# Kernel tuning notes

Hardware: AMD Instinct MI355X
Metric: run time of the kernel (lower is better)

## Reference

```python
import jax, jax.numpy as jnp
import numpy as np

B, H, W, C = 32, 56, 56, 192
WS, SHIFT, NH = 7, 3, 6
HD = C // NH
N = WS * WS
NW = (H // WS) * (W // WS)
HID = 4 * C
EPS = 1e-5


def _np_window_partition(x, ws):
    b, h, w, c = x.shape
    x = x.reshape(b, h // ws, ws, w // ws, ws, c)
    return x.transpose(0, 1, 3, 2, 4, 5).reshape(-1, ws * ws, c)


def build_attn_mask():
    img = np.zeros((1, H, W, 1), dtype=np.float32)
    cnt = 0
    for hs in (slice(0, -WS), slice(-WS, -SHIFT), slice(-SHIFT, None)):
        for ws_ in (slice(0, -WS), slice(-WS, -SHIFT), slice(-SHIFT, None)):
            img[:, hs, ws_, :] = cnt
            cnt += 1
    mw = _np_window_partition(img, WS).squeeze(-1)  # (nW, N)
    am = mw[:, None, :] - mw[:, :, None]
    am = np.where(am != 0, -100.0, 0.0).astype(np.float32)
    return jnp.asarray(am)  # (nW, N, N)


def layernorm(x, g, b):
    mu = jnp.mean(x, axis=-1, keepdims=True)
    var = jnp.var(x, axis=-1, keepdims=True)
    return (x - mu) * jax.lax.rsqrt(var + EPS) * g + b


def setup_inputs() -> dict:
    key = jax.random.key(0)
    ks = jax.random.split(key, 8)
    s = 0.02
    return {
        "x": jax.random.normal(ks[0], (B, H * W, C), dtype=jnp.float32),
        "qkv_w": jax.random.normal(ks[1], (C, 3 * C), dtype=jnp.float32) * s,
        "qkv_b": jnp.zeros((3 * C,), dtype=jnp.float32),
        "proj_w": jax.random.normal(ks[2], (C, C), dtype=jnp.float32) * s,
        "proj_b": jnp.zeros((C,), dtype=jnp.float32),
        "n1_g": jnp.ones((C,), dtype=jnp.float32),
        "n1_b": jnp.zeros((C,), dtype=jnp.float32),
        "n2_g": jnp.ones((C,), dtype=jnp.float32),
        "n2_b": jnp.zeros((C,), dtype=jnp.float32),
        "fc1_w": jax.random.normal(ks[3], (C, HID), dtype=jnp.float32) * s,
        "fc1_b": jnp.zeros((HID,), dtype=jnp.float32),
        "fc2_w": jax.random.normal(ks[4], (HID, C), dtype=jnp.float32) * s,
        "fc2_b": jnp.zeros((C,), dtype=jnp.float32),
        "attn_mask": build_attn_mask(),
    }


def reference(x, qkv_w, qkv_b, proj_w, proj_b, n1_g, n1_b, n2_g, n2_b,
              fc1_w, fc1_b, fc2_w, fc2_b, attn_mask):
    scale = HD ** -0.5
    xv = x.reshape(B, H, W, C)
    shifted = jnp.roll(xv, shift=(-SHIFT, -SHIFT), axis=(1, 2))
    # window partition -> (B*nW, N, C)
    wins = shifted.reshape(B, H // WS, WS, W // WS, WS, C)
    wins = wins.transpose(0, 1, 3, 2, 4, 5).reshape(-1, N, C)
    xn = layernorm(wins, n1_g, n1_b)
    qkv = (xn @ qkv_w + qkv_b).reshape(-1, N, 3, NH, HD)
    q, k, v = qkv[:, :, 0], qkv[:, :, 1], qkv[:, :, 2]  # (B_, N, NH, HD)
    attn = jnp.einsum('bnhd,bmhd->bhnm', q, k) * scale   # (B_, NH, N, N)
    attn = attn.reshape(B, NW, NH, N, N) + attn_mask[None, :, None]
    attn = jax.nn.softmax(attn.reshape(-1, NH, N, N), axis=-1)
    out = jnp.einsum('bhnm,bmhd->bnhd', attn, v).reshape(-1, N, C)
    out = out @ proj_w + proj_b
    # window reverse
    xr = out.reshape(B, H // WS, W // WS, WS, WS, C)
    xr = xr.transpose(0, 1, 3, 2, 4, 5).reshape(B, H, W, C)
    xr = jnp.roll(xr, shift=(SHIFT, SHIFT), axis=(1, 2)).reshape(B, H * W, C)
    # NOTE: no residual around attention (faithful to source); residual only on MLP
    h = layernorm(xr, n2_g, n2_b)
    mlp = jax.nn.gelu(h @ fc1_w + fc1_b, approximate=False) @ fc2_w + fc2_b
    return xr + mlp
```

## Files before the change

### kernel.cpp

```cpp
#include <hip/hip_runtime.h>

typedef unsigned short u16;
typedef unsigned int u32;
typedef __bf16 bf16x8 __attribute__((ext_vector_type(8)));
typedef float f32x4 __attribute__((ext_vector_type(4)));

#define MFMA16(a,b,c) __builtin_amdgcn_mfma_f32_16x16x32_bf16((a),(b),(c),0,0,0)

__device__ __forceinline__ u16 f2bf(float x) {
  u32 u = __float_as_uint(x);
  u32 r = (u + 0x7fffu + ((u >> 16) & 1u)) >> 16;
  return (u16)r;
}

__device__ __forceinline__ float gelu_f(float v) {
  float u = v * 0.70710678118654752f;
  float a = fabsf(u);
  float t = 1.f / (1.f + 0.3275911f * a);
  float p = t * (0.254829592f + t * (-0.284496736f + t * (1.421413741f +
            t * (-1.453152027f + t * 1.061405429f))));
  float e = __expf(-u * u);
  float er = 1.f - p * e;
  er = (u < 0.f) ? -er : er;
  return 0.5f * v * (1.f + er);
}

__global__ __launch_bounds__(256) void prep_weights(
    const float* __restrict__ qkv_w, const float* __restrict__ proj_w,
    const float* __restrict__ fc1_w, const float* __restrict__ fc2_w,
    u16* __restrict__ qkv_wf, u16* __restrict__ proj_wf,
    u16* __restrict__ fc1_wf, u16* __restrict__ fc2_wf) {
  int t0 = blockIdx.x * 256 + threadIdx.x;
  int stride = gridDim.x * 256;
  for (int i = t0; i < 36 * 6 * 512; i += stride) {
    int f = i >> 9, ln = (i >> 3) & 63, e = i & 7;
    int ct = f / 6, kc = f - ct * 6;
    int n = ct * 16 + (ln & 15), k = kc * 32 + (ln >> 4) * 8 + e;
    qkv_wf[i] = f2bf(qkv_w[k * 576 + n]);
  }
  for (int i = t0; i < 12 * 6 * 512; i += stride) {
    int f = i >> 9, ln = (i >> 3) & 63, e = i & 7;
    int ct = f / 6, kc = f - ct * 6;
    int n = ct * 16 + (ln & 15), k = kc * 32 + (ln >> 4) * 8 + e;
    proj_wf[i] = f2bf(proj_w[k * 192 + n]);
  }
  for (int i = t0; i < 48 * 6 * 512; i += stride) {
    int f = i >> 9, ln = (i >> 3) & 63, e = i & 7;
    int ctg = f / 6, kc = f - ctg * 6;
    int n = ctg * 16 + (ln & 15), k = kc * 32 + (ln >> 4) * 8 + e;
    fc1_wf[i] = f2bf(fc1_w[k * 768 + n]);
  }
  for (int i = t0; i < 24 * 12 * 512; i += stride) {
    int f = i >> 9, ln = (i >> 3) & 63, e = i & 7;
    int g2 = f / 12, ct = f - g2 * 12;
    int n = ct * 16 + (ln & 15), k = g2 * 32 + (ln >> 4) * 8 + e;
    fc2_wf[i] = f2bf(fc2_w[k * 192 + n]);
  }
}

__global__ __launch_bounds__(256) void qkv_ln_kernel(
    const float* __restrict__ x, const float* __restrict__ g,
    const float* __restrict__ bb,
    const u16* __restrict__ qkv_wf, const float* __restrict__ qkv_b,
    u16* __restrict__ qkvb, int rowbase, int wbase) {
  __shared__ __align__(16) u16 sA[128 * 200];
  const int tid = threadIdx.x;
  const int r0 = rowbase + blockIdx.x * 128;

  {
    int r = tid >> 1, half = tid & 1;
    int gr = r0 + r;
    int w = gr / 49, n = gr - w * 49;
    int b = w >> 6, wi = w & 63;
    int rr = n / 7, cc = n - rr * 7;
    int hh = (wi >> 3) * 7 + rr + 3; if (hh >= 56) hh -= 56;
    int ww = (wi & 7) * 7 + cc + 3; if (ww >= 56) ww -= 56;
    const float* src = x + ((size_t)b * 3136 + hh * 56 + ww) * 192 + half * 96;
    float s1 = 0.f, s2 = 0.f;
    #pragma unroll
    for (int i = 0; i < 24; i++) {
      float4 v = ((const float4*)src)[i];
      s1 += v.x + v.y + v.z + v.w;
      s2 += v.x * v.x + v.y * v.y + v.z * v.z + v.w * v.w;
    }
    s1 += __shfl_xor(s1, 1);
    s2 += __shfl_xor(s2, 1);
    float mu = s1 * (1.f / 192.f);
    float var = s2 * (1.f / 192.f) - mu * mu;
    float rs = rsqrtf(var + 1e-5f);
    u16* drow = sA + r * 200 + half * 96;
    #pragma unroll
    for (int i = 0; i < 24; i++) {
      float4 v = ((const float4*)src)[i];
      int c = half * 96 + i * 4;
      ushort4 o;
      o.x = f2bf((v.x - mu) * rs * g[c + 0] + bb[c + 0]);
      o.y = f2bf((v.y - mu) * rs * g[c + 1] + bb[c + 1]);
      o.z = f2bf((v.z - mu) * rs * g[c + 2] + bb[c + 2]);
      o.w = f2bf((v.w - mu) * rs * g[c + 3] + bb[c + 3]);
      *((ushort4*)(drow + i * 4)) = o;
    }
  }
  __syncthreads();

  const int wv = tid >> 6, ln = tid & 63, lrow = ln & 15, quad = ln >> 4;
  const int ln8 = ln << 3;

  u32 qkoff[8], voff[8];
  #pragma unroll
  for (int rt = 0; rt < 2; rt++) {
    #pragma unroll
    for (int reg = 0; reg < 4; reg++) {
      int grow = r0 + 32 * wv + 16 * rt + quad * 4 + reg;
      int w_ = grow / 49, n_ = grow - w_ * 49;
      u32 wb = (u32)(w_ - wbase) * 29568u;
      qkoff[rt * 4 + reg] = wb + (u32)n_ * 32u;
      voff[rt * 4 + reg] = wb + (u32)n_;
    }
  }

  for (int ct = 0; ct < 36; ct++) {
    f32x4 acc0 = (f32x4){0.f, 0.f, 0.f, 0.f};
    f32x4 acc1 = (f32x4){0.f, 0.f, 0.f, 0.f};
    #pragma unroll
    for (int kc = 0; kc < 6; kc++) {
      bf16x8 a0 = *(const bf16x8*)(sA + (32 * wv + lrow) * 200 + kc * 32 + quad * 8);
      bf16x8 a1 = *(const bf16x8*)(sA + (32 * wv + 16 + lrow) * 200 + kc * 32 + quad * 8);
      bf16x8 bw = *(const bf16x8*)(qkv_wf + ((ct * 6 + kc) << 9) + ln8);
      acc0 = MFMA16(a0, bw, acc0);
      acc1 = MFMA16(a1, bw, acc1);
    }
    int sec = ct / 12, ccc = ct - sec * 12;
    int head = ccc >> 1, d0 = (ccc & 1) * 16;
    int col = d0 + lrow;
    float bias = qkv_b[sec * 192 + head * 32 + col];
    u32 hoff = (u32)head * 4928u;
    if (sec < 2) {
      u32 coff = hoff + (u32)sec * 1568u + (u32)col;
      #pragma unroll
      for (int reg = 0; reg < 4; reg++) {
        qkvb[qkoff[reg] + coff] = f2bf(acc0[reg] + bias);
        qkvb[qkoff[4 + reg] + coff] = f2bf(acc1[reg] + bias);
      }
    } else {
      u32 coff = hoff + 3136u + (u32)col * 56u;
      #pragma unroll
      for (int reg = 0; reg < 4; reg++) {
        qkvb[voff[reg] + coff] = f2bf(acc0[reg] + bias);
        qkvb[voff[4 + reg] + coff] = f2bf(acc1[reg] + bias);
      }
    }
  }
}

__global__ __launch_bounds__(384) void attn2_kernel(
    const u16* __restrict__ qkvb, u16* __restrict__ attnout, int wbase) {
  __shared__ __align__(16) u16 sP[6 * 64 * 72];
  const int tid = threadIdx.x;
  const int wv = tid >> 6;
  const int ln = tid & 63;
  const int lrow = ln & 15;
  const int quad = ln >> 4;
  const int wl = blockIdx.x;
  const int w = wbase + wl;
  const int wi = w & 63;
  const int wr = wi >> 3, wc = wi & 7;
  const u16* base = qkvb + (size_t)(wl * 6 + wv) * 4928;
  u16* sPw = sP + wv * (64 * 72);
  const f32x4 zero4 = {0.f, 0.f, 0.f, 0.f};

  bf16x8 kf[4];
  #pragma unroll
  for (int rt = 0; rt < 4; rt++)
    kf[rt] = *(const bf16x8*)(base + 1568 + (16 * rt + lrow) * 32 + quad * 8);
  f32x4 S[4][4];
  #pragma unroll
  for (int ct = 0; ct < 4; ct++) {
    bf16x8 qf = *(const bf16x8*)(base + (16 * ct + lrow) * 32 + quad * 8);
    #pragma unroll
    for (int rt = 0; rt < 4; rt++)
      S[rt][ct] = MFMA16(kf[rt], qf, zero4);
  }

  int hbn[4], wbn[4];
  #pragma unroll
  for (int ct = 0; ct < 4; ct++) {
    int n = 16 * ct + lrow;
    int rn = (n * 9363) >> 16;
    int cn = n - 7 * rn;
    hbn[ct] = (wr < 7) ? 0 : ((rn >= 4) ? 2 : 1);
    wbn[ct] = (wc < 7) ? 0 : ((cn >= 4) ? 2 : 1);
  }

  const float scale = 0.17677669529663687f;
  float mx[4] = {-1e30f, -1e30f, -1e30f, -1e30f};
  #pragma unroll
  for (int rt = 0; rt < 4; rt++) {
    #pragma unroll
    for (int reg = 0; reg < 4; reg++) {
      int m = 16 * rt + quad * 4 + reg;
      int rm = (m * 9363) >> 16;
      int cm = m - 7 * rm;
      int hbm = (wr < 7) ? 0 : ((rm >= 4) ? 2 : 1);
      int wbm = (wc < 7) ? 0 : ((cm >= 4) ? 2 : 1);
      bool padm = (m >= 49);
      #pragma unroll
      for (int ct = 0; ct < 4; ct++) {
        float sv = S[rt][ct][reg] * scale +
                   (((hbm != hbn[ct]) || (wbm != wbn[ct])) ? -100.f : 0.f);
        sv = padm ? -1e30f : sv;
        S[rt][ct][reg] = sv;
        mx[ct] = fmaxf(mx[ct], sv);
      }
    }
  }
  #pragma unroll
  for (int ct = 0; ct < 4; ct++) {
    mx[ct] = fmaxf(mx[ct], __shfl_xor(mx[ct], 16));
    mx[ct] = fmaxf(mx[ct], __shfl_xor(mx[ct], 32));
  }
  float sum[4] = {0.f, 0.f, 0.f, 0.f};
  #pragma unroll
  for (int rt = 0; rt < 4; rt++)
    #pragma unroll
    for (int reg = 0; reg < 4; reg++)
      #pragma unroll
      for (int ct = 0; ct < 4; ct++) {
        float e = __expf(S[rt][ct][reg] - mx[ct]);
        S[rt][ct][reg] = e;
        sum[ct] += e;
      }
  float inv[4];
  #pragma unroll
  for (int ct = 0; ct < 4; ct++) {
    sum[ct] += __shfl_xor(sum[ct], 16);
    sum[ct] += __shfl_xor(sum[ct], 32);
    inv[ct] = 1.f / sum[ct];
  }

  #pragma unroll
  for (int rt = 0; rt < 4; rt++) {
    #pragma unroll
    for (int ct = 0; ct < 4; ct++) {
      ushort4 o;
      o.x = f2bf(S[rt][ct][0] * inv[ct]);
      o.y = f2bf(S[rt][ct][1] * inv[ct]);
      o.z = f2bf(S[rt][ct][2] * inv[ct]);
      o.w = f2bf(S[rt][ct][3] * inv[ct]);
      *((ushort4*)(sPw + (16 * ct + lrow) * 72 + 16 * rt + quad * 4)) = o;
    }
  }

  f32x4 accO[4][2];
  #pragma unroll
  for (int rt = 0; rt < 4; rt++)
    #pragma unroll
    for (int cd = 0; cd < 2; cd++) accO[rt][cd] = zero4;
  #pragma unroll
  for (int kc = 0; kc < 2; kc++) {
    bf16x8 vf[2];
    #pragma unroll
    for (int cd = 0; cd < 2; cd++)
      vf[cd] = *(const bf16x8*)(base + 3136 + (16 * cd + lrow) * 56 + kc * 32 + quad * 8);
    #pragma unroll
    for (int rt = 0; rt < 4; rt++) {
      bf16x8 af = *(const bf16x8*)(sPw + (16 * rt + lrow) * 72 + kc * 32 + quad * 8);
      #pragma unroll
      for (int cd = 0; cd < 2; cd++)
        accO[rt][cd] = MFMA16(af, vf[cd], accO[rt][cd]);
    }
  }

  #pragma unroll
  for (int rt = 0; rt < 4; rt++) {
    #pragma unroll
    for (int reg = 0; reg < 4; reg++) {
      int n = 16 * rt + quad * 4 + reg;
      if (n < 49) {
        #pragma unroll
        for (int cd = 0; cd < 2; cd++)
          attnout[(size_t)(w * 49 + n) * 192 + wv * 32 + 16 * cd + lrow] =
              f2bf(accO[rt][cd][reg]);
      }
    }
  }
}

__global__ __launch_bounds__(256, 3) void projmlp_kernel(
    const u16* __restrict__ attnout, const u16* __restrict__ proj_wf,
    const float* __restrict__ proj_b,
    const float* __restrict__ g, const float* __restrict__ bb,
    const u16* __restrict__ fc1_wf, const float* __restrict__ fc1_b,
    const u16* __restrict__ fc2_wf, const float* __restrict__ fc2_b,
    float* __restrict__ out) {
  __shared__ __align__(16) u16 sA[64 * 200];
  __shared__ __align__(16) u16 sT[2 * 64 * 72];
  __shared__ __align__(16) float sStat[64 * 8];
  const int tid = threadIdx.x;
  const int wv = tid >> 6, ln = tid & 63, lrow = ln & 15, quad = ln >> 4;
  const int ln8 = ln << 3;
  const int r0 = blockIdx.x * 64;
  const f32x4 zero4 = {0.f, 0.f, 0.f, 0.f};

  {
    const u32* src = (const u32*)(attnout + (size_t)r0 * 192);
    u32* dst = (u32*)sA;
    #pragma unroll
    for (int i = 0; i < 24; i++) {
      int idx = tid + i * 256;
      int r = idx / 96, c = idx - r * 96;
      dst[r * 100 + c] = src[idx];
    }
  }
  __syncthreads();

  f32x4 xr[4][3];
  #pragma unroll
  for (int rt = 0; rt < 4; rt++)
    #pragma unroll
    for (int ct = 0; ct < 3; ct++) xr[rt][ct] = zero4;
  #pragma unroll
  for (int kc = 0; kc < 6; kc++) {
    bf16x8 af[4];
    #pragma unroll
    for (int rt = 0; rt < 4; rt++)
      af[rt] = *(const bf16x8*)(sA + (16 * rt + lrow) * 200 + kc * 32 + quad * 8);
    #pragma unroll
    for (int ct = 0; ct < 3; ct++) {
      bf16x8 b = *(const bf16x8*)(proj_wf + (((wv * 3 + ct) * 6 + kc) << 9) + ln8);
      #pragma unroll
      for (int rt = 0; rt < 4; rt++)
        xr[rt][ct] = MFMA16(af[rt], b, xr[rt][ct]);
    }
  }
  #pragma unroll
  for (int ct = 0; ct < 3; ct++) {
    float pb = proj_b[wv * 48 + ct * 16 + lrow];
    #pragma unroll
    for (int rt = 0; rt < 4; rt++) {
      xr[rt][ct][0] += pb; xr[rt][ct][1] += pb;
      xr[rt][ct][2] += pb; xr[rt][ct][3] += pb;
    }
  }

  {
    float ps1[4][4], ps2[4][4];
    #pragma unroll
    for (int rt = 0; rt < 4; rt++)
      #pragma unroll
      for (int reg = 0; reg < 4; reg++) {
        float a = xr[rt][0][reg] + xr[rt][1][reg] + xr[rt][2][reg];
        float b = xr[rt][0][reg] * xr[rt][0][reg] +
                  xr[rt][1][reg] * xr[rt][1][reg] +
                  xr[rt][2][reg] * xr[rt][2][reg];
        ps1[rt][reg] = a; ps2[rt][reg] = b;
      }
    #pragma unroll
    for (int m = 1; m <= 8; m <<= 1)
      #pragma unroll
      for (int rt = 0; rt < 4; rt++)
        #pragma unroll
        for (int reg = 0; reg < 4; reg++) {
          ps1[rt][reg] += __shfl_xor(ps1[rt][reg], m);
          ps2[rt][reg] += __shfl_xor(ps2[rt][reg], m);
        }
    if (lrow == 0) {
      #pragma unroll
      for (int rt = 0; rt < 4; rt++)
        #pragma unroll
        for (int reg = 0; reg < 4; reg++) {
          int row = 16 * rt + 4 * quad + reg;
          *(float2*)&sStat[row * 8 + wv * 2] =
              make_float2(ps1[rt][reg], ps2[rt][reg]);
        }
    }
  }
  __syncthreads();

  {
    float gc[3], bc[3];
    #pragma unroll
    for (int ct = 0; ct < 3; ct++) {
      int col = wv * 48 + ct * 16 + lrow;
      gc[ct] = g[col]; bc[ct] = bb[col];
    }
    #pragma unroll
    for (int rt = 0; rt < 4; rt++) {
      float mu_[4], rs_[4];
      #pragma unroll
      for (int reg = 0; reg < 4; reg++) {
        int row = 16 * rt + 4 * quad + reg;
        f32x4 q0 = *(const f32x4*)&sStat[row * 8];
        f32x4 q1 = *(const f32x4*)&sStat[row * 8 + 4];
        float s1 = q0[0] + q0[2] + q1[0] + q1[2];
        float s2 = q0[1] + q0[3] + q1[1] + q1[3];
        float mu = s1 * (1.f / 192.f);
        float var = s2 * (1.f / 192.f) - mu * mu;
        mu_[reg] = mu; rs_[reg] = rsqrtf(var + 1e-5f);
      }
      #pragma unroll
      for (int ct = 0; ct < 3; ct++) {
        int col = wv * 48 + ct * 16 + lrow;
        #pragma unroll
        for (int reg = 0; reg < 4; reg++) {
          int row = 16 * rt + 4 * quad + reg;
          sA[row * 200 + col] =
              f2bf((xr[rt][ct][reg] - mu_[reg]) * rs_[reg] * gc[ct] + bc[ct]);
        }
      }
    }
  }
  __syncthreads();

  f32x4 accO[4][3];
  #pragma unroll
  for (int rt = 0; rt < 4; rt++)
    #pragma unroll
    for (int ct = 0; ct < 3; ct++) accO[rt][ct] = zero4;

  auto FC1 = [&](int ch, u16* dst) {
    f32x4 accT[4] = {zero4, zero4, zero4, zero4};
    #pragma unroll
    for (int kc = 0; kc < 6; kc++) {
      bf16x8 af[4];
      #pragma unroll
      for (int rt = 0; rt < 4; rt++)
        af[rt] = *(const bf16x8*)(sA + (16 * rt + lrow) * 200 + kc * 32 + quad * 8);
      bf16x8 b = *(const bf16x8*)(fc1_wf + (((ch * 4 + wv) * 6 + kc) << 9) + ln8);
      #pragma unroll
      for (int rt = 0; rt < 4; rt++)
        accT[rt] = MFMA16(af[rt], b, accT[rt]);
    }
    float b1 = fc1_b[ch * 64 + wv * 16 + lrow];
    #pragma unroll
    for (int rt = 0; rt < 4; rt++)
      #pragma unroll
      for (int reg = 0; reg < 4; reg++) {
        float v = accT[rt][reg] + b1;
        dst[(16 * rt + 4 * quad + reg) * 72 + wv * 16 + lrow] = f2bf(gelu_f(v));
      }
  };
  auto FC2 = [&](int ch, const u16* src) {
    #pragma unroll
    for (int kc2 = 0; kc2 < 2; kc2++) {
      bf16x8 ta[4];
      #pragma unroll
      for (int rt = 0; rt < 4; rt++)
        ta[rt] = *(const bf16x8*)(src + (16 * rt + lrow) * 72 + kc2 * 32 + quad * 8);
      #pragma unroll
      for (int ct = 0; ct < 3; ct++) {
        bf16x8 b = *(const bf16x8*)(fc2_wf +
            (((ch * 2 + kc2) * 12 + wv * 3 + ct) << 9) + ln8);
        #pragma unroll
        for (int rt = 0; rt < 4; rt++)
          accO[rt][ct] = MFMA16(ta[rt], b, accO[rt][ct]);
      }
    }
  };

  FC1(0, sT);
  __syncthreads();
  for (int ch = 0; ch < 12; ch++) {
    u16* cur = sT + (ch & 1) * (64 * 72);
    u16* nxt = sT + ((ch + 1) & 1) * (64 * 72);
    if (ch < 11) FC1(ch + 1, nxt);
    FC2(ch, cur);
    __syncthreads();
  }

  float fb[3];
  #pragma unroll
  for (int ct = 0; ct < 3; ct++) fb[ct] = fc2_b[wv * 48 + ct * 16 + lrow];
  #pragma unroll
  for (int rt = 0; rt < 4; rt++) {
    #pragma unroll
    for (int reg = 0; reg < 4; reg++) {
      int gr = r0 + 16 * rt + 4 * quad + reg;
      int w = gr / 49, n = gr - w * 49;
      int b = w >> 6, wi = w & 63;
      int rr = n / 7;
      int hh = (wi >> 3) * 7 + rr + 3; if (hh >= 56) hh -= 56;
      int ww = (wi & 7) * 7 + (n - rr * 7) + 3; if (ww >= 56) ww -= 56;
      float* orow = out + ((size_t)b * 3136 + hh * 56 + ww) * 192;
      #pragma unroll
      for (int ct = 0; ct < 3; ct++)
        orow[wv * 48 + ct * 16 + lrow] =
            xr[rt][ct][reg] + accO[rt][ct][reg] + fb[ct];
    }
  }
}

extern "C" void kernel_launch(void* const* d_in, const int* in_sizes, int n_in,
                              void* d_out, int out_size, void* d_ws, size_t ws_size,
                              hipStream_t stream) {
  const float* x      = (const float*)d_in[0];
  const float* qkv_w  = (const float*)d_in[1];
  const float* qkv_b  = (const float*)d_in[2];
  const float* proj_w = (const float*)d_in[3];
  const float* proj_b = (const float*)d_in[4];
  const float* n1_g   = (const float*)d_in[5];
  const float* n1_b   = (const float*)d_in[6];
  const float* n2_g   = (const float*)d_in[7];
  const float* n2_b   = (const float*)d_in[8];
  const float* fc1_w  = (const float*)d_in[9];
  const float* fc1_b  = (const float*)d_in[10];
  const float* fc2_w  = (const float*)d_in[11];
  const float* fc2_b  = (const float*)d_in[12];
  float* out = (float*)d_out;
  char* ws = (char*)d_ws;

  u16* qkvb    = (u16*)(ws + 0);
  u16* attnout = (u16*)(ws + 60555264);
  u16* qkv_wf  = (u16*)(ws + 99090432);
  u16* proj_wf = (u16*)(ws + 99311616);
  u16* fc1_wf  = (u16*)(ws + 99385344);
  u16* fc2_wf  = (u16*)(ws + 99680256);

  prep_weights<<<256, 256, 0, stream>>>(qkv_w, proj_w, fc1_w, fc2_w,
                                        qkv_wf, proj_wf, fc1_wf, fc2_wf);
  for (int hf = 0; hf < 2; hf++) {
    qkv_ln_kernel<<<392, 256, 0, stream>>>(x, n1_g, n1_b, qkv_wf, qkv_b,
                                           qkvb, hf * 50176, hf * 1024);
    attn2_kernel<<<1024, 384, 0, stream>>>(qkvb, attnout, hf * 1024);
  }
  projmlp_kernel<<<1568, 256, 0, stream>>>(attnout, proj_wf, proj_b,
                                           n2_g, n2_b, fc1_wf, fc1_b,
                                           fc2_wf, fc2_b, out);
}
```

Measured before the change: 454.5 us.

## Software-pipeline weight fragment loads into registers in QKV and MLP GEMMs

The QKV kernel now keeps its A fragments in registers and double-buffers the weight fragments for the next column tile, so global loads overlap the MFMAs. The proj/MLP kernel preloads the proj weights and prefetches the fc1/fc2 fragments one chunk ahead. To free the registers that held the residual, it writes the attention residual to the output early and reads it back at the end. Divisions in GELU and softmax become hardware reciprocals. This cuts exposed global-load latency but raises register pressure, which may lower occupancy, and adds an extra read and write of the output.

```diff
diff --git a/kernel.cpp b/kernel.cpp
--- a/kernel.cpp
+++ b/kernel.cpp
@@ -16,7 +16,7 @@
 __device__ __forceinline__ float gelu_f(float v) {
   float u = v * 0.70710678118654752f;
   float a = fabsf(u);
-  float t = 1.f / (1.f + 0.3275911f * a);
+  float t = __builtin_amdgcn_rcpf(1.f + 0.3275911f * a);
   float p = t * (0.254829592f + t * (-0.284496736f + t * (1.421413741f +
             t * (-1.453152027f + t * 1.061405429f))));
   float e = __expf(-u * u);
@@ -58,7 +58,44 @@
   }
 }
 
-__global__ __launch_bounds__(256) void qkv_ln_kernel(
+#define QKV_BODY(CT, CUR, NXT, PF)                                            \
+  {                                                                           \
+    const int ct_ = (CT);                                                     \
+    if (PF) {                                                                 \
+      _Pragma("unroll")                                                       \
+      for (int kc = 0; kc < 6; kc++)                                          \
+        NXT[kc] = *(const bf16x8*)(qkv_wf + (((ct_ + 1) * 6 + kc) << 9) + ln8); \
+      __builtin_amdgcn_sched_barrier(0);                                      \
+    }                                                                         \
+    f32x4 acc0 = zero4, acc1 = zero4;                                         \
+    _Pragma("unroll")                                                         \
+    for (int kc = 0; kc < 6; kc++) {                                          \
+      acc0 = MFMA16(aa0[kc], CUR[kc], acc0);                                  \
+      acc1 = MFMA16(aa1[kc], CUR[kc], acc1);                                  \
+    }                                                                         \
+    int sec = ct_ / 12, ccc = ct_ - sec * 12;                                 \
+    int head = ccc >> 1, d0 = (ccc & 1) * 16;                                 \
+    int col = d0 + lrow;                                                      \
+    float bias = qkv_b[sec * 192 + head * 32 + col];                          \
+    u32 hoff = (u32)head * 4928u;                                             \
+    if (sec < 2) {                                                            \
+      u32 coff = hoff + (u32)sec * 1568u + (u32)col;                          \
+      _Pragma("unroll")                                                       \
+      for (int reg = 0; reg < 4; reg++) {                                     \
+        qkvb[qkoff[reg] + coff] = f2bf(acc0[reg] + bias);                     \
+        qkvb[qkoff[4 + reg] + coff] = f2bf(acc1[reg] + bias);                 \
+      }                                                                       \
+    } else {                                                                  \
+      u32 coff = hoff + 3136u + (u32)col * 56u;                               \
+      _Pragma("unroll")                                                       \
+      for (int reg = 0; reg < 4; reg++) {                                     \
+        qkvb[voff[reg] + coff] = f2bf(acc0[reg] + bias);                      \
+        qkvb[voff[4 + reg] + coff] = f2bf(acc1[reg] + bias);                  \
+      }                                                                       \
+    }                                                                         \
+  }
+
+__global__ __launch_bounds__(256, 3) void qkv_ln_kernel(
     const float* __restrict__ x, const float* __restrict__ g,
     const float* __restrict__ bb,
     const u16* __restrict__ qkv_wf, const float* __restrict__ qkv_b,
@@ -66,6 +103,7 @@
   __shared__ __align__(16) u16 sA[128 * 200];
   const int tid = threadIdx.x;
   const int r0 = rowbase + blockIdx.x * 128;
+  const f32x4 zero4 = {0.f, 0.f, 0.f, 0.f};
 
   {
     int r = tid >> 1, half = tid & 1;
@@ -119,37 +157,21 @@
     }
   }
 
-  for (int ct = 0; ct < 36; ct++) {
-    f32x4 acc0 = (f32x4){0.f, 0.f, 0.f, 0.f};
-    f32x4 acc1 = (f32x4){0.f, 0.f, 0.f, 0.f};
-    #pragma unroll
-    for (int kc = 0; kc < 6; kc++) {
-      bf16x8 a0 = *(const bf16x8*)(sA + (32 * wv + lrow) * 200 + kc * 32 + quad * 8);
-      bf16x8 a1 = *(const bf16x8*)(sA + (32 * wv + 16 + lrow) * 200 + kc * 32 + quad * 8);
-      bf16x8 bw = *(const bf16x8*)(qkv_wf + ((ct * 6 + kc) << 9) + ln8);
-      acc0 = MFMA16(a0, bw, acc0);
-      acc1 = MFMA16(a1, bw, acc1);
-    }
-    int sec = ct / 12, ccc = ct - sec * 12;
-    int head = ccc >> 1, d0 = (ccc & 1) * 16;
-    int col = d0 + lrow;
-    float bias = qkv_b[sec * 192 + head * 32 + col];
-    u32 hoff = (u32)head * 4928u;
-    if (sec < 2) {
-      u32 coff = hoff + (u32)sec * 1568u + (u32)col;
-      #pragma unroll
-      for (int reg = 0; reg < 4; reg++) {
-        qkvb[qkoff[reg] + coff] = f2bf(acc0[reg] + bias);
-        qkvb[qkoff[4 + reg] + coff] = f2bf(acc1[reg] + bias);
-      }
-    } else {
-      u32 coff = hoff + 3136u + (u32)col * 56u;
-      #pragma unroll
-      for (int reg = 0; reg < 4; reg++) {
-        qkvb[voff[reg] + coff] = f2bf(acc0[reg] + bias);
-        qkvb[voff[4 + reg] + coff] = f2bf(acc1[reg] + bias);
-      }
-    }
+  bf16x8 aa0[6], aa1[6];
+  #pragma unroll
+  for (int kc = 0; kc < 6; kc++) {
+    aa0[kc] = *(const bf16x8*)(sA + (32 * wv + lrow) * 200 + kc * 32 + quad * 8);
+    aa1[kc] = *(const bf16x8*)(sA + (32 * wv + 16 + lrow) * 200 + kc * 32 + quad * 8);
+  }
+
+  bf16x8 bwA[6], bwB[6];
+  #pragma unroll
+  for (int kc = 0; kc < 6; kc++)
+    bwA[kc] = *(const bf16x8*)(qkv_wf + (kc << 9) + ln8);
+
+  for (int ctp = 0; ctp < 36; ctp += 2) {
+    QKV_BODY(ctp, bwA, bwB, 1)
+    QKV_BODY(ctp + 1, bwB, bwA, (ctp + 2) < 36)
   }
 }
 
@@ -235,7 +257,7 @@
   for (int ct = 0; ct < 4; ct++) {
     sum[ct] += __shfl_xor(sum[ct], 16);
     sum[ct] += __shfl_xor(sum[ct], 32);
-    inv[ct] = 1.f / sum[ct];
+    inv[ct] = __builtin_amdgcn_rcpf(sum[ct]);
   }
 
   #pragma unroll
@@ -302,6 +324,14 @@
   const int r0 = blockIdx.x * 64;
   const f32x4 zero4 = {0.f, 0.f, 0.f, 0.f};
 
+  bf16x8 pb[18];
+  #pragma unroll
+  for (int ct = 0; ct < 3; ct++)
+    #pragma unroll
+    for (int kc = 0; kc < 6; kc++)
+      pb[ct * 6 + kc] =
+          *(const bf16x8*)(proj_wf + (((wv * 3 + ct) * 6 + kc) << 9) + ln8);
+
   {
     const u32* src = (const u32*)(attnout + (size_t)r0 * 192);
     u32* dst = (u32*)sA;
@@ -326,22 +356,31 @@
     for (int rt = 0; rt < 4; rt++)
       af[rt] = *(const bf16x8*)(sA + (16 * rt + lrow) * 200 + kc * 32 + quad * 8);
     #pragma unroll
-    for (int ct = 0; ct < 3; ct++) {
-      bf16x8 b = *(const bf16x8*)(proj_wf + (((wv * 3 + ct) * 6 + kc) << 9) + ln8);
+    for (int ct = 0; ct < 3; ct++)
       #pragma unroll
       for (int rt = 0; rt < 4; rt++)
-        xr[rt][ct] = MFMA16(af[rt], b, xr[rt][ct]);
-    }
+        xr[rt][ct] = MFMA16(af[rt], pb[ct * 6 + kc], xr[rt][ct]);
   }
   #pragma unroll
   for (int ct = 0; ct < 3; ct++) {
-    float pb = proj_b[wv * 48 + ct * 16 + lrow];
+    float pbias = proj_b[wv * 48 + ct * 16 + lrow];
     #pragma unroll
     for (int rt = 0; rt < 4; rt++) {
-      xr[rt][ct][0] += pb; xr[rt][ct][1] += pb;
-      xr[rt][ct][2] += pb; xr[rt][ct][3] += pb;
-    }
-  }
+      xr[rt][ct][0] += pbias; xr[rt][ct][1] += pbias;
+      xr[rt][ct][2] += pbias; xr[rt][ct][3] += pbias;
+    }
+  }
+
+  bf16x8 fc1b[6], fc2b[6];
+  #pragma unroll
+  for (int kc = 0; kc < 6; kc++)
+    fc1b[kc] = *(const bf16x8*)(fc1_wf + (((0 * 4 + wv) * 6 + kc) << 9) + ln8);
+  #pragma unroll
+  for (int kc2 = 0; kc2 < 2; kc2++)
+    #pragma unroll
+    for (int ct = 0; ct < 3; ct++)
+      fc2b[kc2 * 3 + ct] = *(const bf16x8*)(fc2_wf +
+          (((0 * 2 + kc2) * 12 + wv * 3 + ct) << 9) + ln8);
 
   {
     float ps1[4][4], ps2[4][4];
@@ -408,6 +447,19 @@
               f2bf((xr[rt][ct][reg] - mu_[reg]) * rs_[reg] * gc[ct] + bc[ct]);
         }
       }
+      #pragma unroll
+      for (int reg = 0; reg < 4; reg++) {
+        int gr = r0 + 16 * rt + 4 * quad + reg;
+        int w = gr / 49, n = gr - w * 49;
+        int b = w >> 6, wi = w & 63;
+        int rr = n / 7;
+        int hh = (wi >> 3) * 7 + rr + 3; if (hh >= 56) hh -= 56;
+        int ww = (wi & 7) * 7 + (n - rr * 7) + 3; if (ww >= 56) ww -= 56;
+        float* orow = out + ((size_t)b * 3136 + hh * 56 + ww) * 192;
+        #pragma unroll
+        for (int ct = 0; ct < 3; ct++)
+          orow[wv * 48 + ct * 16 + lrow] = xr[rt][ct][reg];
+      }
     }
   }
   __syncthreads();
@@ -426,10 +478,9 @@
       #pragma unroll
       for (int rt = 0; rt < 4; rt++)
         af[rt] = *(const bf16x8*)(sA + (16 * rt + lrow) * 200 + kc * 32 + quad * 8);
-      bf16x8 b = *(const bf16x8*)(fc1_wf + (((ch * 4 + wv) * 6 + kc) << 9) + ln8);
       #pragma unroll
       for (int rt = 0; rt < 4; rt++)
-        accT[rt] = MFMA16(af[rt], b, accT[rt]);
+        accT[rt] = MFMA16(af[rt], fc1b[kc], accT[rt]);
     }
     float b1 = fc1_b[ch * 64 + wv * 16 + lrow];
     #pragma unroll
@@ -440,7 +491,7 @@
         dst[(16 * rt + 4 * quad + reg) * 72 + wv * 16 + lrow] = f2bf(gelu_f(v));
       }
   };
-  auto FC2 = [&](int ch, const u16* src) {
+  auto FC2 = [&](const u16* src) {
     #pragma unroll
     for (int kc2 = 0; kc2 < 2; kc2++) {
       bf16x8 ta[4];
@@ -448,23 +499,35 @@
       for (int rt = 0; rt < 4; rt++)
         ta[rt] = *(const bf16x8*)(src + (16 * rt + lrow) * 72 + kc2 * 32 + quad * 8);
       #pragma unroll
-      for (int ct = 0; ct < 3; ct++) {
-        bf16x8 b = *(const bf16x8*)(fc2_wf +
-            (((ch * 2 + kc2) * 12 + wv * 3 + ct) << 9) + ln8);
+      for (int ct = 0; ct < 3; ct++)
         #pragma unroll
         for (int rt = 0; rt < 4; rt++)
-          accO[rt][ct] = MFMA16(ta[rt], b, accO[rt][ct]);
-      }
+          accO[rt][ct] = MFMA16(ta[rt], fc2b[kc2 * 3 + ct], accO[rt][ct]);
     }
   };
 
   FC1(0, sT);
   __syncthreads();
   for (int ch = 0; ch < 12; ch++) {
-    u16* cur = sT + (ch & 1) * (64 * 72);
+    if (ch < 11) {
+      #pragma unroll
+      for (int kc = 0; kc < 6; kc++)
+        fc1b[kc] = *(const bf16x8*)(fc1_wf +
+            ((((ch + 1) * 4 + wv) * 6 + kc) << 9) + ln8);
+      __builtin_amdgcn_sched_barrier(0);
+    }
+    const u16* cur = sT + (ch & 1) * (64 * 72);
     u16* nxt = sT + ((ch + 1) & 1) * (64 * 72);
-    if (ch < 11) FC1(ch + 1, nxt);
-    FC2(ch, cur);
+    FC2(cur);
+    if (ch < 11) {
+      #pragma unroll
+      for (int kc2 = 0; kc2 < 2; kc2++)
+        #pragma unroll
+        for (int ct = 0; ct < 3; ct++)
+          fc2b[kc2 * 3 + ct] = *(const bf16x8*)(fc2_wf +
+              ((((ch + 1) * 2 + kc2) * 12 + wv * 3 + ct) << 9) + ln8);
+      FC1(ch + 1, nxt);
+    }
     __syncthreads();
   }
 
@@ -483,9 +546,10 @@
       int ww = (wi & 7) * 7 + (n - rr * 7) + 3; if (ww >= 56) ww -= 56;
       float* orow = out + ((size_t)b * 3136 + hh * 56 + ww) * 192;
       #pragma unroll
-      for (int ct = 0; ct < 3; ct++)
-        orow[wv * 48 + ct * 16 + lrow] =
-            xr[rt][ct][reg] + accO[rt][ct][reg] + fb[ct];
+      for (int ct = 0; ct < 3; ct++) {
+        int col = wv * 48 + ct * 16 + lrow;
+        orow[col] = orow[col] + accO[rt][ct][reg] + fb[ct];
+      }
     }
   }
 }
```

Result: no change. 463.5 us (+2.0%).

## Prefetch MLP and proj weight fragments into registers ahead of use

Applied to the files above, without the earlier changes.

The projection/MLP kernel now loads all proj weight fragments up front into registers, and in the FC1/FC2 chunk loop it issues the next chunk's fc1 and fc2 weight loads before the current MFMA work, reordering FC2 before FC1 so global loads overlap compute. Separately, two divisions (GELU and softmax normalization) become hardware reciprocal approximations. This aims to hide global weight-load latency, at the cost of many more live VGPRs under a 3-blocks-per-SM launch bound, which may cause spills or lower occupancy.

```diff
diff --git a/kernel.cpp b/kernel.cpp
--- a/kernel.cpp
+++ b/kernel.cpp
@@ -16,7 +16,7 @@
 __device__ __forceinline__ float gelu_f(float v) {
   float u = v * 0.70710678118654752f;
   float a = fabsf(u);
-  float t = 1.f / (1.f + 0.3275911f * a);
+  float t = __builtin_amdgcn_rcpf(1.f + 0.3275911f * a);
   float p = t * (0.254829592f + t * (-0.284496736f + t * (1.421413741f +
             t * (-1.453152027f + t * 1.061405429f))));
   float e = __expf(-u * u);
@@ -235,7 +235,7 @@
   for (int ct = 0; ct < 4; ct++) {
     sum[ct] += __shfl_xor(sum[ct], 16);
     sum[ct] += __shfl_xor(sum[ct], 32);
-    inv[ct] = 1.f / sum[ct];
+    inv[ct] = __builtin_amdgcn_rcpf(sum[ct]);
   }
 
   #pragma unroll
@@ -302,6 +302,14 @@
   const int r0 = blockIdx.x * 64;
   const f32x4 zero4 = {0.f, 0.f, 0.f, 0.f};
 
+  bf16x8 pb[18];
+  #pragma unroll
+  for (int ct = 0; ct < 3; ct++)
+    #pragma unroll
+    for (int kc = 0; kc < 6; kc++)
+      pb[ct * 6 + kc] =
+          *(const bf16x8*)(proj_wf + (((wv * 3 + ct) * 6 + kc) << 9) + ln8);
+
   {
     const u32* src = (const u32*)(attnout + (size_t)r0 * 192);
     u32* dst = (u32*)sA;
@@ -326,22 +334,31 @@
     for (int rt = 0; rt < 4; rt++)
       af[rt] = *(const bf16x8*)(sA + (16 * rt + lrow) * 200 + kc * 32 + quad * 8);
     #pragma unroll
-    for (int ct = 0; ct < 3; ct++) {
-      bf16x8 b = *(const bf16x8*)(proj_wf + (((wv * 3 + ct) * 6 + kc) << 9) + ln8);
+    for (int ct = 0; ct < 3; ct++)
       #pragma unroll
       for (int rt = 0; rt < 4; rt++)
-        xr[rt][ct] = MFMA16(af[rt], b, xr[rt][ct]);
-    }
+        xr[rt][ct] = MFMA16(af[rt], pb[ct * 6 + kc], xr[rt][ct]);
   }
   #pragma unroll
   for (int ct = 0; ct < 3; ct++) {
-    float pb = proj_b[wv * 48 + ct * 16 + lrow];
+    float pbias = proj_b[wv * 48 + ct * 16 + lrow];
     #pragma unroll
     for (int rt = 0; rt < 4; rt++) {
-      xr[rt][ct][0] += pb; xr[rt][ct][1] += pb;
-      xr[rt][ct][2] += pb; xr[rt][ct][3] += pb;
-    }
-  }
+      xr[rt][ct][0] += pbias; xr[rt][ct][1] += pbias;
+      xr[rt][ct][2] += pbias; xr[rt][ct][3] += pbias;
+    }
+  }
+
+  bf16x8 fc1b[6], fc2b[6];
+  #pragma unroll
+  for (int kc = 0; kc < 6; kc++)
+    fc1b[kc] = *(const bf16x8*)(fc1_wf + (((0 * 4 + wv) * 6 + kc) << 9) + ln8);
+  #pragma unroll
+  for (int kc2 = 0; kc2 < 2; kc2++)
+    #pragma unroll
+    for (int ct = 0; ct < 3; ct++)
+      fc2b[kc2 * 3 + ct] = *(const bf16x8*)(fc2_wf +
+          (((0 * 2 + kc2) * 12 + wv * 3 + ct) << 9) + ln8);
 
   {
     float ps1[4][4], ps2[4][4];
@@ -426,10 +443,9 @@
       #pragma unroll
       for (int rt = 0; rt < 4; rt++)
         af[rt] = *(const bf16x8*)(sA + (16 * rt + lrow) * 200 + kc * 32 + quad * 8);
-      bf16x8 b = *(const bf16x8*)(fc1_wf + (((ch * 4 + wv) * 6 + kc) << 9) + ln8);
       #pragma unroll
       for (int rt = 0; rt < 4; rt++)
-        accT[rt] = MFMA16(af[rt], b, accT[rt]);
+        accT[rt] = MFMA16(af[rt], fc1b[kc], accT[rt]);
     }
     float b1 = fc1_b[ch * 64 + wv * 16 + lrow];
     #pragma unroll
@@ -440,7 +456,7 @@
         dst[(16 * rt + 4 * quad + reg) * 72 + wv * 16 + lrow] = f2bf(gelu_f(v));
       }
   };
-  auto FC2 = [&](int ch, const u16* src) {
+  auto FC2 = [&](const u16* src) {
     #pragma unroll
     for (int kc2 = 0; kc2 < 2; kc2++) {
       bf16x8 ta[4];
@@ -448,23 +464,35 @@
       for (int rt = 0; rt < 4; rt++)
         ta[rt] = *(const bf16x8*)(src + (16 * rt + lrow) * 72 + kc2 * 32 + quad * 8);
       #pragma unroll
-      for (int ct = 0; ct < 3; ct++) {
-        bf16x8 b = *(const bf16x8*)(fc2_wf +
-            (((ch * 2 + kc2) * 12 + wv * 3 + ct) << 9) + ln8);
+      for (int ct = 0; ct < 3; ct++)
         #pragma unroll
         for (int rt = 0; rt < 4; rt++)
-          accO[rt][ct] = MFMA16(ta[rt], b, accO[rt][ct]);
-      }
+          accO[rt][ct] = MFMA16(ta[rt], fc2b[kc2 * 3 + ct], accO[rt][ct]);
     }
   };
 
   FC1(0, sT);
   __syncthreads();
   for (int ch = 0; ch < 12; ch++) {
-    u16* cur = sT + (ch & 1) * (64 * 72);
+    if (ch < 11) {
+      #pragma unroll
+      for (int kc = 0; kc < 6; kc++)
+        fc1b[kc] = *(const bf16x8*)(fc1_wf +
+            ((((ch + 1) * 4 + wv) * 6 + kc) << 9) + ln8);
+      __builtin_amdgcn_sched_barrier(0);
+    }
+    const u16* cur = sT + (ch & 1) * (64 * 72);
     u16* nxt = sT + ((ch + 1) & 1) * (64 * 72);
-    if (ch < 11) FC1(ch + 1, nxt);
-    FC2(ch, cur);
+    FC2(cur);
+    if (ch < 11) {
+      #pragma unroll
+      for (int kc2 = 0; kc2 < 2; kc2++)
+        #pragma unroll
+        for (int ct = 0; ct < 3; ct++)
+          fc2b[kc2 * 3 + ct] = *(const bf16x8*)(fc2_wf +
+              ((((ch + 1) * 2 + kc2) * 12 + wv * 3 + ct) << 9) + ln8);
+      FC1(ch + 1, nxt);
+    }
     __syncthreads();
   }
 
@@ -483,9 +511,10 @@
       int ww = (wi & 7) * 7 + (n - rr * 7) + 3; if (ww >= 56) ww -= 56;
       float* orow = out + ((size_t)b * 3136 + hh * 56 + ww) * 192;
       #pragma unroll
-      for (int ct = 0; ct < 3; ct++)
-        orow[wv * 48 + ct * 16 + lrow] =
-            xr[rt][ct][reg] + accO[rt][ct][reg] + fb[ct];
+      for (int ct = 0; ct < 3; ct++) {
+        int col = wv * 48 + ct * 16 + lrow;
+        orow[col] = xr[rt][ct][reg] + accO[rt][ct][reg] + fb[ct];
+      }
     }
   }
 }
```

Result: slower. 464.4 us (+2.2%).
